# Kernel optimization log

Measured on AMD Instinct MI355X. Metric: run time of the kernel, lower is better.

Reference implementation:

```python
import jax, jax.numpy as jnp
import numpy as np

GRID = 256

def _build_edges(g):
    ii, jj = np.meshgrid(np.arange(g), np.arange(g), indexing='ij')
    center = ii * g + jj
    srcs, tgts, attrs = [], [], []
    for di in (-1, 0, 1):
        for dj in (-1, 0, 1):
            if di == 0 and dj == 0:
                continue
            ni, nj = ii + di, jj + dj
            m = (ni >= 0) & (ni < g) & (nj >= 0) & (nj < g)
            srcs.append(center[m])
            tgts.append((ni * g + nj)[m])
            n = int(m.sum())
            a = np.empty((n, 3), np.float32)
            a[:, 0] = np.sqrt(di * di + dj * dj)
            a[:, 1] = di
            a[:, 2] = dj
            attrs.append(a)
    return (np.concatenate(srcs).astype(np.int32),
            np.concatenate(tgts).astype(np.int32),
            np.concatenate(attrs, axis=0))

def setup_inputs() -> dict:
    key = jax.random.key(0)
    ks = jax.random.split(key, 16)
    B, T, C, g = 2, 5, 10, GRID
    width, kw, out_c, Hh = 64, 32, 10, 32
    src, tgt, attr = _build_edges(g)
    nrm = lambda k, s: 0.1 * jax.random.normal(k, s, dtype=jnp.float32)
    return {
        'x': nrm(ks[0], (B, T, C, g, g)),
        'edge_src': jnp.asarray(src),
        'edge_tgt': jnp.asarray(tgt),
        'edge_attr': jnp.asarray(attr),
        'Wih0': nrm(ks[1], (4 * Hh, C)),
        'Whh0': nrm(ks[2], (4 * Hh, Hh)),
        'bih0': nrm(ks[3], (4 * Hh,)),
        'bhh0': nrm(ks[4], (4 * Hh,)),
        'Wih1': nrm(ks[5], (4 * Hh, Hh)),
        'Whh1': nrm(ks[6], (4 * Hh, Hh)),
        'bih1': nrm(ks[7], (4 * Hh,)),
        'bhh1': nrm(ks[8], (4 * Hh,)),
        'fc1_w': nrm(ks[9], (width, Hh)),
        'fc1_b': nrm(ks[10], (width,)),
        'conv_w': nrm(ks[11], (4, width, width)),
        'conv_b': nrm(ks[12], (4, width)),
        'gparam': jnp.ones((4,), jnp.float32),
        'fc2_w': nrm(ks[13], (kw, width)),
        'fc2_b': nrm(ks[14], (kw,)),
        'fc3_w': nrm(ks[15], (out_c, kw)),
        'fc3_b': jnp.zeros((out_c,), jnp.float32),
    }

def _lstm_cell(xt, h, c, Wih, Whh, bih, bhh):
    z = xt @ Wih.T + bih + h @ Whh.T + bhh
    i, f, g, o = jnp.split(z, 4, axis=-1)  # torch gate order i,f,g,o
    c = jax.nn.sigmoid(f) * c + jax.nn.sigmoid(i) * jnp.tanh(g)
    h = jax.nn.sigmoid(o) * jnp.tanh(c)
    return h, c

def _forward(x, edge_src, edge_tgt, edge_attr, Wih0, Whh0, bih0, bhh0,
             Wih1, Whh1, bih1, bhh1, fc1_w, fc1_b, conv_w, conv_b, gparam,
             fc2_w, fc2_b, fc3_w, fc3_b):
    B, T, C, H, W = x.shape
    N = H * W
    Hh = Whh0.shape[1]
    # (B,T,C,H,W) -> (T, B*N, C) sequence for the temporal LSTM over every node
    seq = x.transpose(0, 3, 4, 1, 2).reshape(B * N, T, C).transpose(1, 0, 2)

    def step(carry, xt):
        h0, c0, h1, c1 = carry
        h0, c0 = _lstm_cell(xt, h0, c0, Wih0, Whh0, bih0, bhh0)
        h1, c1 = _lstm_cell(h0, h1, c1, Wih1, Whh1, bih1, bhh1)
        return (h0, c0, h1, c1), None

    z = jnp.zeros((B * N, Hh), x.dtype)
    (h0, c0, h1, c1), _ = jax.lax.scan(step, (z, z, z, z), seq)
    feats = jax.nn.relu(h1 @ fc1_w.T + fc1_b).reshape(B, N, -1)  # (B,N,width)

    dist2 = edge_attr[:, 0:1] ** 2  # (E,1)
    depth = conv_w.shape[0]
    for k in range(depth):
        gw = jnp.exp(-dist2 / (gparam[k] ** 2 + 1e-8))       # (E,1) gaussian gate
        msg = (feats[:, edge_src] @ conv_w[k]) * gw          # (B,E,width)
        agg = jnp.zeros_like(feats).at[:, edge_tgt].add(msg) # scatter-add per batch
        feats = agg + feats @ conv_w[k] + conv_b[k]
        if k != depth - 1:
            feats = jax.nn.relu(feats)

    out = jax.nn.relu(feats @ fc2_w.T + fc2_b) @ fc3_w.T + fc3_b  # (B,N,out_c)
    out = out.reshape(B, H, W, -1).transpose(0, 3, 1, 2)[:, None]  # (B,1,out_c,H,W)
    return out

def reference(x, edge_src, edge_tgt, edge_attr, Wih0, Whh0, bih0, bhh0,
              Wih1, Whh1, bih1, bhh1, fc1_w, fc1_b, conv_w, conv_b, gparam,
              fc2_w, fc2_b, fc3_w, fc3_b):
    return _forward(x, edge_src, edge_tgt, edge_attr, Wih0, Whh0, bih0, bhh0,
                    Wih1, Whh1, bih1, bhh1, fc1_w, fc1_b, conv_w, conv_b, gparam,
                    fc2_w, fc2_b, fc3_w, fc3_b)
```

## Files before the change

### kernel.cpp

```cpp
#include <hip/hip_runtime.h>
#include <hip/hip_bf16.h>

#define NPIX   65536
#define TT     5
#define CC     10
#define HH     32
#define WIDTH  64
#define KW     32
#define OUTC   10

#define OFF_L0I    0
#define OFF_L0H    1280
#define OFF_L1I    5376
#define OFF_L1H    9472
#define OFF_B0     13568
#define OFF_B1     13696
#define OFF_FC1W   13824
#define OFF_FC1B   15872
#define OFF_CWT2   16384
#define OFF_CB     32768
#define OFF_FC2W2  33024
#define OFF_FC2B   35072
#define OFF_FC3W4  35104
#define OFF_FC3B   35424
#define OFF_GW     35440
#define OFF_FEATS_A 36864
#define OFF_FEATS_B (36864 + 8388608)

#define STRAIGHT_ATTR_IDX (65025 * 3)

__device__ __forceinline__ float sigf(float x)  { return 1.0f / (1.0f + __expf(-x)); }
__device__ __forceinline__ float tanhf_(float x){ return 1.0f - 2.0f / (__expf(2.0f * x) + 1.0f); }

__global__ __launch_bounds__(256, 1)
void prep_kernel(const float* Wih0, const float* Whh0,
                 const float* bih0, const float* bhh0,
                 const float* Wih1, const float* Whh1,
                 const float* bih1, const float* bhh1,
                 const float* fc1w, const float* fc1b,
                 const float* convw, const float* convb,
                 const float* fc2w, const float* fc2b,
                 const float* fc3w, const float* fc3b,
                 const float* gparam, const float* eattr,
                 float* P) {
    int tid = blockIdx.x * blockDim.x + threadIdx.x;
    int stride = gridDim.x * blockDim.x;
    for (int idx = tid; idx < 1280; idx += stride) {
        int g = idx & 3, j = (idx >> 2) & 31, c = idx >> 7;
        P[OFF_L0I + idx] = Wih0[(g * 32 + j) * 10 + c];
    }
    for (int idx = tid; idx < 4096; idx += stride) {
        int g = idx & 3, j = (idx >> 2) & 31, k = idx >> 7;
        P[OFF_L0H + idx] = Whh0[(g * 32 + j) * 32 + k];
        P[OFF_L1I + idx] = Wih1[(g * 32 + j) * 32 + k];
        P[OFF_L1H + idx] = Whh1[(g * 32 + j) * 32 + k];
    }
    for (int idx = tid; idx < 128; idx += stride) {
        int g = idx & 3, j = idx >> 2;
        P[OFF_B0 + idx] = bih0[g * 32 + j] + bhh0[g * 32 + j];
        P[OFF_B1 + idx] = bih1[g * 32 + j] + bhh1[g * 32 + j];
    }
    for (int idx = tid; idx < 2048; idx += stride) {
        int ch = idx & 63, k = idx >> 6;
        P[OFF_FC1W + idx] = fc1w[ch * 32 + k];
    }
    for (int i = tid; i < 64; i += stride) P[OFF_FC1B + i] = fc1b[i];
    for (int idx = tid; idx < 16384; idx += stride)
        P[OFF_CWT2 + idx] = convw[idx];
    for (int i = tid; i < 256; i += stride) P[OFF_CB + i] = convb[i];
    for (int idx = tid; idx < 2048; idx += stride) {
        int e = idx >> 1, h = idx & 1, m2 = e >> 6, ch = e & 63;
        P[OFF_FC2W2 + idx] = fc2w[(2 * m2 + h) * 64 + ch];
    }
    for (int i = tid; i < 32;  i += stride) P[OFF_FC2B + i] = fc2b[i];
    for (int idx = tid; idx < 320; idx += stride) {
        int q = idx & 3, e = idx >> 2, oc2 = e >> 4, m2 = e & 15;
        int oc = 2 * oc2 + (q & 1), m = 2 * m2 + (q >> 1);
        P[OFF_FC3W4 + idx] = fc3w[oc * 32 + m];
    }
    for (int i = tid; i < 10; i += stride) P[OFF_FC3B + i] = fc3b[i];
    for (int idx = tid; idx < 8; idx += stride) {
        int k = idx >> 1;
        float g = gparam[k];
        float denom = g * g + 1e-8f;
        float a = (idx & 1) ? eattr[0] : eattr[STRAIGHT_ATTR_IDX];
        P[OFF_GW + idx] = __expf(-(a * a) / denom);
    }
}

#define ROW_ACC32(WBASE, SVAL) do {                                 \
    const float* wr_ = (WBASE); float sv_ = (SVAL);                 \
    _Pragma("unroll")                                               \
    for (int q_ = 0; q_ < 32; q_++)                                 \
        z[q_] = __builtin_fmaf(wr_[q_], sv_, z[q_]);                \
    } while (0)

__global__ __launch_bounds__(256, 1)
void lstm_fc1_kernel(const float* __restrict__ x,
                     const float* __restrict__ P,
                     float* __restrict__ feats) {
    __shared__ float H0[HH * 64];
    __shared__ float H1[HH * 64];

    int tid  = threadIdx.x;
    int w    = __builtin_amdgcn_readfirstlane(tid >> 6);
    int lane = tid & 63;
    int jw   = w << 3;
    int w32  = w << 5;

    int n = blockIdx.x * 64 + lane;
    int b = n >> 16;
    int pix = n & (NPIX - 1);
    const float* xb = x + (size_t)b * TT * CC * NPIX + pix;

    float c0[8], c1[8];
#pragma unroll
    for (int j = 0; j < 8; j++) {
        c0[j] = 0.f; c1[j] = 0.f;
        H0[(jw + j) * 64 + lane] = 0.f;
        H1[(jw + j) * 64 + lane] = 0.f;
    }
    __syncthreads();

#pragma unroll 1
    for (int t = 0; t < TT; t++) {
        float xcur[CC];
#pragma unroll
        for (int c = 0; c < CC; c++)
            xcur[c] = xb[(size_t)(t * CC + c) * NPIX];

        {
            float z[32];
            const float* bb = P + OFF_B0 + w32;
#pragma unroll
            for (int q = 0; q < 32; q++) z[q] = bb[q];
#pragma unroll 1
            for (int c = 0; c < CC; c++)
                ROW_ACC32(P + OFF_L0I + c * 128 + w32, xcur[c]);
#pragma unroll 1
            for (int k = 0; k < HH; k++) {
                float hv = H0[k * 64 + lane];
                ROW_ACC32(P + OFF_L0H + k * 128 + w32, hv);
            }
            __syncthreads();
#pragma unroll
            for (int j = 0; j < 8; j++) {
                float cn = sigf(z[4 * j + 1]) * c0[j]
                         + sigf(z[4 * j + 0]) * tanhf_(z[4 * j + 2]);
                c0[j] = cn;
                H0[(jw + j) * 64 + lane] = sigf(z[4 * j + 3]) * tanhf_(cn);
            }
            __syncthreads();
        }

        {
            float z[32];
            const float* bb = P + OFF_B1 + w32;
#pragma unroll
            for (int q = 0; q < 32; q++) z[q] = bb[q];
#pragma unroll 1
            for (int k = 0; k < HH; k++) {
                float hv = H0[k * 64 + lane];
                ROW_ACC32(P + OFF_L1I + k * 128 + w32, hv);
            }
#pragma unroll 1
            for (int k = 0; k < HH; k++) {
                float hv = H1[k * 64 + lane];
                ROW_ACC32(P + OFF_L1H + k * 128 + w32, hv);
            }
            __syncthreads();
#pragma unroll
            for (int j = 0; j < 8; j++) {
                float cn = sigf(z[4 * j + 1]) * c1[j]
                         + sigf(z[4 * j + 0]) * tanhf_(z[4 * j + 2]);
                c1[j] = cn;
                H1[(jw + j) * 64 + lane] = sigf(z[4 * j + 3]) * tanhf_(cn);
            }
            __syncthreads();
        }
    }

    float f[16];
    {
        const float* fb1 = P + OFF_FC1B + (w << 4);
#pragma unroll
        for (int m = 0; m < 16; m++) f[m] = fb1[m];
    }
#pragma unroll 1
    for (int k = 0; k < HH; k++) {
        float hv = H1[k * 64 + lane];
        const float* wr = P + OFF_FC1W + k * 64 + (w << 4);
#pragma unroll
        for (int m = 0; m < 16; m++)
            f[m] = __builtin_fmaf(wr[m], hv, f[m]);
    }
    float* fob = feats + (size_t)b * WIDTH * NPIX + (size_t)(w * 16) * NPIX + pix;
#pragma unroll
    for (int m = 0; m < 16; m++)
        fob[(size_t)m * NPIX] = fmaxf(f[m], 0.f);
}

__global__ __launch_bounds__(256, 1)
void conv_fused_kernel(const float* __restrict__ Fin, float* __restrict__ Fout,
                       const float* __restrict__ P, int k) {
    __shared__ float US[64 * 256];
    __shared__ float CW[64 * 64];

    int tid = threadIdx.x;
    {
        const float4* src = (const float4*)(P + OFF_CWT2 + k * 4096);
        float4* dst = (float4*)CW;
        for (int idx = tid; idx < 1024; idx += 256) dst[idx] = src[idx];
    }

    int n = blockIdx.x * 256 + tid;
    int b = n >> 16;
    int pix = n & (NPIX - 1);
    int i = pix >> 8, j = pix & 255;
    float wstr = P[OFF_GW + 2 * k], wdiag = P[OFF_GW + 2 * k + 1];
    float fu = (i > 0) ? wstr : 0.f, fd = (i < 255) ? wstr : 0.f;
    float fl = (j > 0) ? wstr : 0.f, fr = (j < 255) ? wstr : 0.f;
    float ful = (i > 0 && j > 0) ? wdiag : 0.f, fur = (i > 0 && j < 255) ? wdiag : 0.f;
    float fdl = (i < 255 && j > 0) ? wdiag : 0.f, fdr = (i < 255 && j < 255) ? wdiag : 0.f;

    const float* fb = Fin + (size_t)b * WIDTH * NPIX + pix;
#pragma unroll
    for (int ch = 0; ch < WIDTH; ch++) {
        const float* yc = fb + (size_t)ch * NPIX;
        float v = yc[0];
        v += fu * yc[-256] + fd * yc[256] + fl * yc[-1] + fr * yc[1];
        v += ful * yc[-257] + fur * yc[-255] + fdl * yc[255] + fdr * yc[257];
        US[ch * 256 + tid] = v;
    }
    __syncthreads();

    int l = tid & 63;
    int ob16 = (tid >> 6) << 4;
    float4 acc[16];
#pragma unroll
    for (int o = 0; o < 16; o++) {
        float bv = P[OFF_CB + k * 64 + ob16 + o];
        acc[o] = make_float4(bv, bv, bv, bv);
    }
    const float4* US4 = (const float4*)US;
#pragma unroll 2
    for (int ci = 0; ci < 64; ci++) {
        float4 u4 = US4[ci * 64 + l];
        const float4* wr4 = (const float4*)(CW + ci * 64 + ob16);
#pragma unroll
        for (int q = 0; q < 4; q++) {
            float4 wq = wr4[q];
            acc[4 * q + 0].x = __builtin_fmaf(wq.x, u4.x, acc[4 * q + 0].x);
            acc[4 * q + 0].y = __builtin_fmaf(wq.x, u4.y, acc[4 * q + 0].y);
            acc[4 * q + 0].z = __builtin_fmaf(wq.x, u4.z, acc[4 * q + 0].z);
            acc[4 * q + 0].w = __builtin_fmaf(wq.x, u4.w, acc[4 * q + 0].w);
            acc[4 * q + 1].x = __builtin_fmaf(wq.y, u4.x, acc[4 * q + 1].x);
            acc[4 * q + 1].y = __builtin_fmaf(wq.y, u4.y, acc[4 * q + 1].y);
            acc[4 * q + 1].z = __builtin_fmaf(wq.y, u4.z, acc[4 * q + 1].z);
            acc[4 * q + 1].w = __builtin_fmaf(wq.y, u4.w, acc[4 * q + 1].w);
            acc[4 * q + 2].x = __builtin_fmaf(wq.z, u4.x, acc[4 * q + 2].x);
            acc[4 * q + 2].y = __builtin_fmaf(wq.z, u4.y, acc[4 * q + 2].y);
            acc[4 * q + 2].z = __builtin_fmaf(wq.z, u4.z, acc[4 * q + 2].z);
            acc[4 * q + 2].w = __builtin_fmaf(wq.z, u4.w, acc[4 * q + 2].w);
            acc[4 * q + 3].x = __builtin_fmaf(wq.w, u4.x, acc[4 * q + 3].x);
            acc[4 * q + 3].y = __builtin_fmaf(wq.w, u4.y, acc[4 * q + 3].y);
            acc[4 * q + 3].z = __builtin_fmaf(wq.w, u4.z, acc[4 * q + 3].z);
            acc[4 * q + 3].w = __builtin_fmaf(wq.w, u4.w, acc[4 * q + 3].w);
        }
    }

    int pn = blockIdx.x * 256 + 4 * l;
    int pb = pn >> 16;
    int ppix = pn & (NPIX - 1);
    float* ob = Fout + (size_t)pb * WIDTH * NPIX + ppix;
#pragma unroll
    for (int o = 0; o < 16; o++) {
        float4 r;
        r.x = fmaxf(acc[o].x, 0.f); r.y = fmaxf(acc[o].y, 0.f);
        r.z = fmaxf(acc[o].z, 0.f); r.w = fmaxf(acc[o].w, 0.f);
        *(float4*)(ob + (size_t)(ob16 + o) * NPIX) = r;
    }
}

__global__ __launch_bounds__(256, 1)
void conv_head_kernel(const float* __restrict__ Fin, const float* __restrict__ P,
                      float* __restrict__ out) {
    const int k = 3;
    __shared__ float4 CW3[1024];
    __shared__ float  CB3[64];
    __shared__ float4 F2W[512];
    __shared__ float  F2B[32];
    __shared__ float4 F3W[80];
    __shared__ float  F3B[12];
    {
        const float* wsrc = P + OFF_CWT2 + k * 4096;
        for (int idx = threadIdx.x; idx < 1024; idx += 256) {
            int co2 = idx >> 5, ci2 = idx & 31;
            CW3[idx] = make_float4(wsrc[(2 * ci2) * 64 + 2 * co2],
                                   wsrc[(2 * ci2) * 64 + 2 * co2 + 1],
                                   wsrc[(2 * ci2 + 1) * 64 + 2 * co2],
                                   wsrc[(2 * ci2 + 1) * 64 + 2 * co2 + 1]);
        }
        const float4* s2 = (const float4*)(P + OFF_FC2W2);
        for (int i = threadIdx.x; i < 512; i += 256) F2W[i] = s2[i];
        const float4* s3 = (const float4*)(P + OFF_FC3W4);
        if (threadIdx.x < 80) F3W[threadIdx.x] = s3[threadIdx.x];
        if (threadIdx.x < 64) CB3[threadIdx.x] = P[OFF_CB + k * 64 + threadIdx.x];
        if (threadIdx.x < 32) F2B[threadIdx.x] = P[OFF_FC2B + threadIdx.x];
        if (threadIdx.x < 10) F3B[threadIdx.x] = P[OFF_FC3B + threadIdx.x];
    }
    __syncthreads();

    int n = blockIdx.x * 256 + threadIdx.x;
    int b = n >> 16;
    int pix = n & (NPIX - 1);
    int i = pix >> 8, j = pix & 255;
    float wstr = P[OFF_GW + 2 * k], wdiag = P[OFF_GW + 2 * k + 1];
    float fu = (i > 0) ? wstr : 0.f, fd = (i < 255) ? wstr : 0.f;
    float fl = (j > 0) ? wstr : 0.f, fr = (j < 255) ? wstr : 0.f;
    float ful = (i > 0 && j > 0) ? wdiag : 0.f, fur = (i > 0 && j < 255) ? wdiag : 0.f;
    float fdl = (i < 255 && j > 0) ? wdiag : 0.f, fdr = (i < 255 && j < 255) ? wdiag : 0.f;

    const float* fb = Fin + (size_t)b * WIDTH * NPIX + pix;
    float u[WIDTH];
#pragma unroll
    for (int ch = 0; ch < WIDTH; ch++) {
        const float* yc = fb + (size_t)ch * NPIX;
        float v = yc[0];
        v += fu * yc[-256] + fd * yc[256] + fl * yc[-1] + fr * yc[1];
        v += ful * yc[-257] + fur * yc[-255] + fdl * yc[255] + fdr * yc[257];
        u[ch] = v;
    }

    float f[WIDTH];
#pragma unroll
    for (int co2 = 0; co2 < 32; co2++) {
        float ax = CB3[2 * co2], ay = CB3[2 * co2 + 1];
        const float4* wv = CW3 + co2 * 32;
#pragma unroll
        for (int ci2 = 0; ci2 < 32; ci2++) {
            float4 q = wv[ci2];
            float a0 = u[2 * ci2], a1 = u[2 * ci2 + 1];
            ax = __builtin_fmaf(q.x, a0, ax); ax = __builtin_fmaf(q.z, a1, ax);
            ay = __builtin_fmaf(q.y, a0, ay); ay = __builtin_fmaf(q.w, a1, ay);
        }
        f[2 * co2] = ax; f[2 * co2 + 1] = ay;
    }

    float2 oo[5];
#pragma unroll
    for (int oc2 = 0; oc2 < 5; oc2++) oo[oc2] = make_float2(F3B[2 * oc2], F3B[2 * oc2 + 1]);
#pragma unroll 1
    for (int m2 = 0; m2 < 16; m2++) {
        float ax = F2B[2 * m2], ay = F2B[2 * m2 + 1];
        const float4* wv = F2W + m2 * 32;
#pragma unroll
        for (int ch2 = 0; ch2 < 32; ch2++) {
            float4 q = wv[ch2];
            ax = __builtin_fmaf(q.x, f[2 * ch2], ax); ax = __builtin_fmaf(q.z, f[2 * ch2 + 1], ax);
            ay = __builtin_fmaf(q.y, f[2 * ch2], ay); ay = __builtin_fmaf(q.w, f[2 * ch2 + 1], ay);
        }
        ax = fmaxf(ax, 0.f); ay = fmaxf(ay, 0.f);
#pragma unroll
        for (int oc2 = 0; oc2 < 5; oc2++) {
            float4 q = F3W[oc2 * 16 + m2];
            oo[oc2].x += q.x * ax + q.z * ay;
            oo[oc2].y += q.y * ax + q.w * ay;
        }
    }
    float* ob = out + (size_t)b * OUTC * NPIX + pix;
#pragma unroll
    for (int oc2 = 0; oc2 < 5; oc2++) {
        ob[(size_t)(2 * oc2) * NPIX]     = oo[oc2].x;
        ob[(size_t)(2 * oc2 + 1) * NPIX] = oo[oc2].y;
    }
}

extern "C" void kernel_launch(void* const* d_in, const int* in_sizes, int n_in,
                              void* d_out, int out_size, void* d_ws, size_t ws_size,
                              hipStream_t stream) {
    const float* x     = (const float*)d_in[0];
    const float* eattr = (const float*)d_in[3];
    const float* Wih0  = (const float*)d_in[4];
    const float* Whh0  = (const float*)d_in[5];
    const float* bih0  = (const float*)d_in[6];
    const float* bhh0  = (const float*)d_in[7];
    const float* Wih1  = (const float*)d_in[8];
    const float* Whh1  = (const float*)d_in[9];
    const float* bih1  = (const float*)d_in[10];
    const float* bhh1  = (const float*)d_in[11];
    const float* fc1w  = (const float*)d_in[12];
    const float* fc1b  = (const float*)d_in[13];
    const float* convw = (const float*)d_in[14];
    const float* convb = (const float*)d_in[15];
    const float* gparam= (const float*)d_in[16];
    const float* fc2w  = (const float*)d_in[17];
    const float* fc2b  = (const float*)d_in[18];
    const float* fc3w  = (const float*)d_in[19];
    const float* fc3b  = (const float*)d_in[20];

    float* P  = (float*)d_ws;
    float* FA = P + OFF_FEATS_A;
    float* FB = P + OFF_FEATS_B;

    prep_kernel<<<64, 256, 0, stream>>>(Wih0, Whh0, bih0, bhh0, Wih1, Whh1, bih1, bhh1,
                                        fc1w, fc1b, convw, convb, fc2w, fc2b, fc3w, fc3b,
                                        gparam, eattr, P);
    lstm_fc1_kernel<<<2048, 256, 0, stream>>>(x, P, FA);
    conv_fused_kernel<<<512, 256, 0, stream>>>(FA, FB, P, 0);
    conv_fused_kernel<<<512, 256, 0, stream>>>(FB, FA, P, 1);
    conv_fused_kernel<<<512, 256, 0, stream>>>(FA, FB, P, 2);
    conv_head_kernel<<<512, 256, 0, stream>>>(FB, P, (float*)d_out);
}
```

Before: 563.5 us.

## Stage stencil output in shared memory and register-tile the final conv matmul

```diff
diff --git a/kernel.cpp b/kernel.cpp
--- a/kernel.cpp
+++ b/kernel.cpp
@@ -286,32 +286,17 @@
 void conv_head_kernel(const float* __restrict__ Fin, const float* __restrict__ P,
                       float* __restrict__ out) {
     const int k = 3;
-    __shared__ float4 CW3[1024];
-    __shared__ float  CB3[64];
-    __shared__ float4 F2W[512];
-    __shared__ float  F2B[32];
-    __shared__ float4 F3W[80];
-    __shared__ float  F3B[12];
+    __shared__ float US[64 * 256];
+    __shared__ float CW[64 * 64];
+
+    int tid = threadIdx.x;
     {
-        const float* wsrc = P + OFF_CWT2 + k * 4096;
-        for (int idx = threadIdx.x; idx < 1024; idx += 256) {
-            int co2 = idx >> 5, ci2 = idx & 31;
-            CW3[idx] = make_float4(wsrc[(2 * ci2) * 64 + 2 * co2],
-                                   wsrc[(2 * ci2) * 64 + 2 * co2 + 1],
-                                   wsrc[(2 * ci2 + 1) * 64 + 2 * co2],
-                                   wsrc[(2 * ci2 + 1) * 64 + 2 * co2 + 1]);
-        }
-        const float4* s2 = (const float4*)(P + OFF_FC2W2);
-        for (int i = threadIdx.x; i < 512; i += 256) F2W[i] = s2[i];
-        const float4* s3 = (const float4*)(P + OFF_FC3W4);
-        if (threadIdx.x < 80) F3W[threadIdx.x] = s3[threadIdx.x];
-        if (threadIdx.x < 64) CB3[threadIdx.x] = P[OFF_CB + k * 64 + threadIdx.x];
-        if (threadIdx.x < 32) F2B[threadIdx.x] = P[OFF_FC2B + threadIdx.x];
-        if (threadIdx.x < 10) F3B[threadIdx.x] = P[OFF_FC3B + threadIdx.x];
-    }
-    __syncthreads();
-
-    int n = blockIdx.x * 256 + threadIdx.x;
+        const float4* src = (const float4*)(P + OFF_CWT2 + k * 4096);
+        float4* dst = (float4*)CW;
+        for (int idx = tid; idx < 1024; idx += 256) dst[idx] = src[idx];
+    }
+
+    int n = blockIdx.x * 256 + tid;
     int b = n >> 16;
     int pix = n & (NPIX - 1);
     int i = pix >> 8, j = pix & 255;
@@ -321,31 +306,76 @@
     float ful = (i > 0 && j > 0) ? wdiag : 0.f, fur = (i > 0 && j < 255) ? wdiag : 0.f;
     float fdl = (i < 255 && j > 0) ? wdiag : 0.f, fdr = (i < 255 && j < 255) ? wdiag : 0.f;
 
-    const float* fb = Fin + (size_t)b * WIDTH * NPIX + pix;
-    float u[WIDTH];
+    const float* fbp = Fin + (size_t)b * WIDTH * NPIX + pix;
 #pragma unroll
     for (int ch = 0; ch < WIDTH; ch++) {
-        const float* yc = fb + (size_t)ch * NPIX;
+        const float* yc = fbp + (size_t)ch * NPIX;
         float v = yc[0];
         v += fu * yc[-256] + fd * yc[256] + fl * yc[-1] + fr * yc[1];
         v += ful * yc[-257] + fur * yc[-255] + fdl * yc[255] + fdr * yc[257];
-        u[ch] = v;
-    }
+        US[ch * 256 + tid] = v;
+    }
+    __syncthreads();
+
+    int l = tid & 63;
+    int ob16 = (tid >> 6) << 4;
+    float4 acc[16];
+#pragma unroll
+    for (int o = 0; o < 16; o++) {
+        float bv = P[OFF_CB + k * 64 + ob16 + o];
+        acc[o] = make_float4(bv, bv, bv, bv);
+    }
+    const float4* US4 = (const float4*)US;
+#pragma unroll 2
+    for (int ci = 0; ci < 64; ci++) {
+        float4 u4 = US4[ci * 64 + l];
+        const float4* wr4 = (const float4*)(CW + ci * 64 + ob16);
+#pragma unroll
+        for (int q = 0; q < 4; q++) {
+            float4 wq = wr4[q];
+            acc[4 * q + 0].x = __builtin_fmaf(wq.x, u4.x, acc[4 * q + 0].x);
+            acc[4 * q + 0].y = __builtin_fmaf(wq.x, u4.y, acc[4 * q + 0].y);
+            acc[4 * q + 0].z = __builtin_fmaf(wq.x, u4.z, acc[4 * q + 0].z);
+            acc[4 * q + 0].w = __builtin_fmaf(wq.x, u4.w, acc[4 * q + 0].w);
+            acc[4 * q + 1].x = __builtin_fmaf(wq.y, u4.x, acc[4 * q + 1].x);
+            acc[4 * q + 1].y = __builtin_fmaf(wq.y, u4.y, acc[4 * q + 1].y);
+            acc[4 * q + 1].z = __builtin_fmaf(wq.y, u4.z, acc[4 * q + 1].z);
+            acc[4 * q + 1].w = __builtin_fmaf(wq.y, u4.w, acc[4 * q + 1].w);
+            acc[4 * q + 2].x = __builtin_fmaf(wq.z, u4.x, acc[4 * q + 2].x);
+            acc[4 * q + 2].y = __builtin_fmaf(wq.z, u4.y, acc[4 * q + 2].y);
+            acc[4 * q + 2].z = __builtin_fmaf(wq.z, u4.z, acc[4 * q + 2].z);
+            acc[4 * q + 2].w = __builtin_fmaf(wq.z, u4.w, acc[4 * q + 2].w);
+            acc[4 * q + 3].x = __builtin_fmaf(wq.w, u4.x, acc[4 * q + 3].x);
+            acc[4 * q + 3].y = __builtin_fmaf(wq.w, u4.y, acc[4 * q + 3].y);
+            acc[4 * q + 3].z = __builtin_fmaf(wq.w, u4.z, acc[4 * q + 3].z);
+            acc[4 * q + 3].w = __builtin_fmaf(wq.w, u4.w, acc[4 * q + 3].w);
+        }
+    }
+    __syncthreads();
+
+#pragma unroll
+    for (int o = 0; o < 16; o++)
+        *(float4*)&US[(ob16 + o) * 256 + 4 * l] = acc[o];
+    {
+        float4* f2w = (float4*)CW;
+        const float4* s2 = (const float4*)(P + OFF_FC2W2);
+        for (int idx = tid; idx < 512; idx += 256) f2w[idx] = s2[idx];
+        float4* f3w = (float4*)(CW + 2048);
+        const float4* s3 = (const float4*)(P + OFF_FC3W4);
+        if (tid < 80) f3w[tid] = s3[tid];
+        if (tid < 32) CW[2048 + 320 + tid] = P[OFF_FC2B + tid];
+        if (tid < 10) CW[2048 + 352 + tid] = P[OFF_FC3B + tid];
+    }
+    __syncthreads();
 
     float f[WIDTH];
 #pragma unroll
-    for (int co2 = 0; co2 < 32; co2++) {
-        float ax = CB3[2 * co2], ay = CB3[2 * co2 + 1];
-        const float4* wv = CW3 + co2 * 32;
-#pragma unroll
-        for (int ci2 = 0; ci2 < 32; ci2++) {
-            float4 q = wv[ci2];
-            float a0 = u[2 * ci2], a1 = u[2 * ci2 + 1];
-            ax = __builtin_fmaf(q.x, a0, ax); ax = __builtin_fmaf(q.z, a1, ax);
-            ay = __builtin_fmaf(q.y, a0, ay); ay = __builtin_fmaf(q.w, a1, ay);
-        }
-        f[2 * co2] = ax; f[2 * co2 + 1] = ay;
-    }
+    for (int ch = 0; ch < WIDTH; ch++) f[ch] = US[ch * 256 + tid];
+
+    const float4* F2W = (const float4*)CW;
+    const float4* F3W = (const float4*)(CW + 2048);
+    const float*  F2B = CW + 2048 + 320;
+    const float*  F3B = CW + 2048 + 352;
 
     float2 oo[5];
 #pragma unroll
```

After: 529.4 us. 6.1% less time.
